# Kernel optimization log

Measured on AMD Instinct MI355X. Metric: run time of the kernel, lower is better.

Reference implementation:

```python
import jax, jax.numpy as jnp
import numpy as np

M_FAI = 1024


def _cmul_mm(a, b):
    # complex matmul of (2, M, M) @ (2, M, M) -> (2, M, M)
    re = a[0] @ b[0] - a[1] @ b[1]
    im = a[0] @ b[1] + a[1] @ b[0]
    return jnp.stack([re, im])


def _cmul_el(a, b):
    # elementwise complex multiply, leading dim 2 = (real, imag)
    re = a[0] * b[0] - a[1] * b[1]
    im = a[0] * b[1] + a[1] * b[0]
    return jnp.stack([re, im])


def _diag(x):
    # diagonal of (2, M, M) -> (2, M)
    return jnp.diagonal(x, axis1=1, axis2=2)


def setup_inputs() -> dict:
    key = jax.random.key(0)
    ks = jax.random.split(key, 13)
    mats = {}
    names = ['Theta', 'A1', 'B1', 'C1', 'A2', 'B2', 'C2', 'A3', 'B3', 'C3']
    for i, n in enumerate(names):
        mats[n] = jax.random.normal(ks[i], (2, M_FAI, M_FAI), dtype=jnp.float32)
    mats['alpha'] = jnp.ones((1,), dtype=jnp.float32)
    mats['belta'] = jnp.ones((1,), dtype=jnp.float32)
    # xavier_uniform with gain=0.01 on (2, M_fai): bound = 0.01*sqrt(6/(2+M_fai))
    bound = 0.01 * np.sqrt(6.0 / (2 + M_FAI))
    mats['param1'] = jax.random.uniform(ks[10], (2, M_FAI), dtype=jnp.float32, minval=-bound, maxval=bound)
    mats['param2'] = jax.random.uniform(ks[11], (2, M_FAI), dtype=jnp.float32, minval=-bound, maxval=bound)
    return mats


def reference(Theta, A1, B1, C1, A2, B2, C2, A3, B3, C3, alpha, belta, param1, param2):
    # approximateTheta = cdiag(param1); diag(p) @ C == columnwise complex scale of C rows
    p = param1[:, :, None]  # (2, M, 1)
    Q1 = _cmul_mm(A1, _cmul_el(p, C1))
    Q2 = _cmul_mm(A2, _cmul_el(p, C2))
    Q3 = _cmul_mm(A2, _cmul_el(p, C3))  # original uses A2 here (faithful)

    Thd = _diag(Theta)  # (2, M)
    b1 = alpha * _cmul_el(_diag(A1), _cmul_el(Thd, _diag(C1))) - _diag(Q1) + _diag(B1)
    b2 = belta * _cmul_el(_diag(A2), _cmul_el(Thd, _diag(C2))) - _diag(Q2) + _diag(B2)
    b3 = belta * _cmul_el(_diag(A3), _cmul_el(Thd, _diag(C3))) - _diag(Q3) + _diag(B3)
    b = b1 + b2 + b3 + param2  # (2, M)
    # per-column complex unit-normalize: torch.norm over the (2,1) column
    norm = jnp.sqrt(jnp.sum(b * b, axis=0, keepdims=True))
    theta_new = b / norm  # (2, M)
    # cdiag: embed as (2, M, M) diagonal complex matrix
    Theta_new = jax.vmap(jnp.diag)(theta_new)
    return Theta_new
```

## Files before the change

kernel.cpp:

```cpp
#include <hip/hip_runtime.h>
#include <math.h>

#define M 1024

#define TI 64
#define KCH 16
#define KSPLIT 16
#define KB (M / KSPLIT)

__global__ __launch_bounds__(256)
void diagq_kernel(const float* __restrict__ A1, const float* __restrict__ C1,
                  const float* __restrict__ A2, const float* __restrict__ C2,
                  const float* __restrict__ C3, const float* __restrict__ p1,
                  float* __restrict__ D )
{
    __shared__ float As_re[TI][KCH + 1];
    __shared__ float As_im[TI][KCH + 1];
    __shared__ float Cs_re[KCH][TI];
    __shared__ float Cs_im[KCH][TI];
    __shared__ float red_re[256];
    __shared__ float red_im[256];

    const int t  = threadIdx.x;
    const int i0 = blockIdx.x * TI;
    const int q  = blockIdx.y;
    const int k0 = blockIdx.z * KB;

    const float* __restrict__ A = (q == 0) ? A1 : A2;
    const float* __restrict__ C = (q == 0) ? C1 : ((q == 1) ? C2 : C3);

    const int i_local = t & 63;
    const int kslice  = t >> 6;

    const int a_ii = t >> 2;
    const int a_kk = (t & 3) << 2;
    const int c_kk = t >> 4;
    const int c_ii = (t & 15) << 2;

    const size_t MM = (size_t)M * M;

    float acc_re = 0.f, acc_im = 0.f;

    for (int s = 0; s < KB / KCH; ++s) {
        const int kbase = k0 + s * KCH;

        {
            const size_t row = (size_t)(i0 + a_ii) * M + kbase + a_kk;
            const float4 are = *(const float4*)(A + row);
            const float4 aim = *(const float4*)(A + MM + row);
            As_re[a_ii][a_kk + 0] = are.x;
            As_re[a_ii][a_kk + 1] = are.y;
            As_re[a_ii][a_kk + 2] = are.z;
            As_re[a_ii][a_kk + 3] = are.w;
            As_im[a_ii][a_kk + 0] = aim.x;
            As_im[a_ii][a_kk + 1] = aim.y;
            As_im[a_ii][a_kk + 2] = aim.z;
            As_im[a_ii][a_kk + 3] = aim.w;
        }
        {
            const int k = kbase + c_kk;
            const float pre = p1[k];
            const float pim = p1[M + k];
            const size_t row = (size_t)k * M + i0 + c_ii;
            const float4 cre = *(const float4*)(C + row);
            const float4 cim = *(const float4*)(C + MM + row);
            Cs_re[c_kk][c_ii + 0] = pre * cre.x - pim * cim.x;
            Cs_re[c_kk][c_ii + 1] = pre * cre.y - pim * cim.y;
            Cs_re[c_kk][c_ii + 2] = pre * cre.z - pim * cim.z;
            Cs_re[c_kk][c_ii + 3] = pre * cre.w - pim * cim.w;
            Cs_im[c_kk][c_ii + 0] = pre * cim.x + pim * cre.x;
            Cs_im[c_kk][c_ii + 1] = pre * cim.y + pim * cre.y;
            Cs_im[c_kk][c_ii + 2] = pre * cim.z + pim * cre.z;
            Cs_im[c_kk][c_ii + 3] = pre * cim.w + pim * cre.w;
        }
        __syncthreads();

        #pragma unroll
        for (int j = 0; j < 4; ++j) {
            const int kk = (kslice << 2) + j;
            const float a_re = As_re[i_local][kk];
            const float a_im = As_im[i_local][kk];
            const float c_re = Cs_re[kk][i_local];
            const float c_im = Cs_im[kk][i_local];
            acc_re += a_re * c_re - a_im * c_im;
            acc_im += a_re * c_im + a_im * c_re;
        }
        __syncthreads();
    }

    red_re[t] = acc_re;
    red_im[t] = acc_im;
    __syncthreads();
    if (t < 64) {
        const float sr = red_re[t] + red_re[t + 64] + red_re[t + 128] + red_re[t + 192];
        const float si = red_im[t] + red_im[t + 64] + red_im[t + 128] + red_im[t + 192];
        atomicAdd(&D[(q * 2 + 0) * M + i0 + t], sr);
        atomicAdd(&D[(q * 2 + 1) * M + i0 + t], si);
    }
}

__global__ __launch_bounds__(256)
void finalize_kernel(const float* __restrict__ Theta,
                     const float* __restrict__ A1, const float* __restrict__ B1, const float* __restrict__ C1,
                     const float* __restrict__ A2, const float* __restrict__ B2, const float* __restrict__ C2,
                     const float* __restrict__ A3, const float* __restrict__ B3, const float* __restrict__ C3,
                     const float* __restrict__ alpha, const float* __restrict__ belta,
                     const float* __restrict__ p2, const float* __restrict__ D,
                     float* __restrict__ out)
{
    const int i = blockIdx.x * blockDim.x + threadIdx.x;
    if (i >= M) return;
    const size_t MM = (size_t)M * M;
    const size_t dg = (size_t)i * M + i;

    const float th_re = Theta[dg], th_im = Theta[MM + dg];
    const float al = alpha[0], be = belta[0];

    float b_re = p2[i], b_im = p2[M + i];

    {
        const float a_re = A1[dg], a_im = A1[MM + dg];
        const float c_re = C1[dg], c_im = C1[MM + dg];
        const float t_re = th_re * c_re - th_im * c_im;
        const float t_im = th_re * c_im + th_im * c_re;
        const float u_re = a_re * t_re - a_im * t_im;
        const float u_im = a_re * t_im + a_im * t_re;
        b_re += al * u_re - D[0 * M + i] + B1[dg];
        b_im += al * u_im - D[1 * M + i] + B1[MM + dg];
    }
    {
        const float a_re = A2[dg], a_im = A2[MM + dg];
        const float c_re = C2[dg], c_im = C2[MM + dg];
        const float t_re = th_re * c_re - th_im * c_im;
        const float t_im = th_re * c_im + th_im * c_re;
        const float u_re = a_re * t_re - a_im * t_im;
        const float u_im = a_re * t_im + a_im * t_re;
        b_re += be * u_re - D[2 * M + i] + B2[dg];
        b_im += be * u_im - D[3 * M + i] + B2[MM + dg];
    }
    {
        const float a_re = A3[dg], a_im = A3[MM + dg];
        const float c_re = C3[dg], c_im = C3[MM + dg];
        const float t_re = th_re * c_re - th_im * c_im;
        const float t_im = th_re * c_im + th_im * c_re;
        const float u_re = a_re * t_re - a_im * t_im;
        const float u_im = a_re * t_im + a_im * t_re;
        b_re += be * u_re - D[4 * M + i] + B3[dg];
        b_im += be * u_im - D[5 * M + i] + B3[MM + dg];
    }

    const float inv = 1.0f / sqrtf(b_re * b_re + b_im * b_im);
    out[dg]      = b_re * inv;
    out[MM + dg] = b_im * inv;
}

extern "C" void kernel_launch(void* const* d_in, const int* in_sizes, int n_in,
                              void* d_out, int out_size, void* d_ws, size_t ws_size,
                              hipStream_t stream) {
    const float* Theta = (const float*)d_in[0];
    const float* A1    = (const float*)d_in[1];
    const float* B1    = (const float*)d_in[2];
    const float* C1    = (const float*)d_in[3];
    const float* A2    = (const float*)d_in[4];
    const float* B2    = (const float*)d_in[5];
    const float* C2    = (const float*)d_in[6];
    const float* A3    = (const float*)d_in[7];
    const float* B3    = (const float*)d_in[8];
    const float* C3    = (const float*)d_in[9];
    const float* alpha = (const float*)d_in[10];
    const float* belta = (const float*)d_in[11];
    const float* p1    = (const float*)d_in[12];
    const float* p2    = (const float*)d_in[13];
    float* out = (float*)d_out;
    float* D   = (float*)d_ws;

    hipMemsetAsync(d_out, 0, (size_t)out_size * sizeof(float), stream);
    hipMemsetAsync(d_ws, 0, 6 * M * sizeof(float), stream);

    dim3 grid(M / TI, 3, KSPLIT);
    diagq_kernel<<<grid, 256, 0, stream>>>(A1, C1, A2, C2, C3, p1, D);

    finalize_kernel<<<dim3(M / 256), 256, 0, stream>>>(
        Theta, A1, B1, C1, A2, B2, C2, A3, B3, C3, alpha, belta, p2, D, out);
}
```

Measured before the change: 136.0 us.

## Fuse output zeroing into finalize, replace atomics with split partials, retile

Removes both hipMemsetAsync calls. The finalize kernel now runs one block per row: it zeroes that row of the output and writes the diagonal element. The diagonal-product kernel writes per-K-split partial sums to the workspace instead of using atomicAdd, and finalize reduces those partials. The tile changes to 32 rows with a K-chunk of 32. This trades launch and memset overhead plus atomics for a larger finalize grid and more workspace traffic.

Measured after the change: 130.5 us. 1.04x faster.

```diff
diff --git a/kernel.cpp b/kernel.cpp
--- a/kernel.cpp
+++ b/kernel.cpp
@@ -3,8 +3,8 @@
 
 #define M 1024
 
-#define TI 64
-#define KCH 16
+#define TI 32
+#define KCH 32
 #define KSPLIT 16
 #define KB (M / KSPLIT)
 
@@ -24,54 +24,50 @@
     const int t  = threadIdx.x;
     const int i0 = blockIdx.x * TI;
     const int q  = blockIdx.y;
-    const int k0 = blockIdx.z * KB;
+    const int z  = blockIdx.z;
+    const int k0 = z * KB;
 
     const float* __restrict__ A = (q == 0) ? A1 : A2;
     const float* __restrict__ C = (q == 0) ? C1 : ((q == 1) ? C2 : C3);
 
-    const int i_local = t & 63;
-    const int kslice  = t >> 6;
-
-    const int a_ii = t >> 2;
-    const int a_kk = (t & 3) << 2;
-    const int c_kk = t >> 4;
-    const int c_ii = (t & 15) << 2;
-
     const size_t MM = (size_t)M * M;
 
+    const int l_row = t >> 3;
+    const int l_c4  = (t & 7) << 2;
+
+    const int i_local = t & 31;
+    const int kslice  = t >> 5;
+
     float acc_re = 0.f, acc_im = 0.f;
 
+    #pragma unroll
     for (int s = 0; s < KB / KCH; ++s) {
         const int kbase = k0 + s * KCH;
 
         {
-            const size_t row = (size_t)(i0 + a_ii) * M + kbase + a_kk;
-            const float4 are = *(const float4*)(A + row);
-            const float4 aim = *(const float4*)(A + MM + row);
-            As_re[a_ii][a_kk + 0] = are.x;
-            As_re[a_ii][a_kk + 1] = are.y;
-            As_re[a_ii][a_kk + 2] = are.z;
-            As_re[a_ii][a_kk + 3] = are.w;
-            As_im[a_ii][a_kk + 0] = aim.x;
-            As_im[a_ii][a_kk + 1] = aim.y;
-            As_im[a_ii][a_kk + 2] = aim.z;
-            As_im[a_ii][a_kk + 3] = aim.w;
-        }
-        {
-            const int k = kbase + c_kk;
+            const size_t off = (size_t)(i0 + l_row) * M + kbase + l_c4;
+            const float4 are = *(const float4*)(A + off);
+            const float4 aim = *(const float4*)(A + MM + off);
+            As_re[l_row][l_c4 + 0] = are.x; As_re[l_row][l_c4 + 1] = are.y;
+            As_re[l_row][l_c4 + 2] = are.z; As_re[l_row][l_c4 + 3] = are.w;
+            As_im[l_row][l_c4 + 0] = aim.x; As_im[l_row][l_c4 + 1] = aim.y;
+            As_im[l_row][l_c4 + 2] = aim.z; As_im[l_row][l_c4 + 3] = aim.w;
+        }
+        {
+            const int k = kbase + l_row;
             const float pre = p1[k];
             const float pim = p1[M + k];
-            const size_t row = (size_t)k * M + i0 + c_ii;
-            const float4 cre = *(const float4*)(C + row);
-            const float4 cim = *(const float4*)(C + MM + row);
-            Cs_re[c_kk][c_ii + 0] = pre * cre.x - pim * cim.x;
-            Cs_re[c_kk][c_ii + 1] = pre * cre.y - pim * cim.y;
-            Cs_re[c_kk][c_ii + 2] = pre * cre.z - pim * cim.z;
-            Cs_re[c_kk][c_ii + 3] = pre * cre.w - pim * cim.w;
-            Cs_im[c_kk][c_ii + 0] = pre * cim.x + pim * cre.x;
-            Cs_im[c_kk][c_ii + 1] = pre * cim.y + pim * cre.y;
-            Cs_im[c_kk][c_ii + 2] = pre * cim.z + pim * cre.z;
-            Cs_im[c_kk][c_ii + 3] = pre * cim.w + pim * cre.w;
+            const size_t off = (size_t)k * M + i0 + l_c4;
+            const float4 cre = *(const float4*)(C + off);
+            const float4 cim = *(const float4*)(C + MM + off);
+            Cs_re[l_row][l_c4 + 0] = pre * cre.x - pim * cim.x;
+            Cs_re[l_row][l_c4 + 1] = pre * cre.y - pim * cim.y;
+            Cs_re[l_row][l_c4 + 2] = pre * cre.z - pim * cim.z;
+            Cs_re[l_row][l_c4 + 3] = pre * cre.w - pim * cim.w;
+            Cs_im[l_row][l_c4 + 0] = pre * cim.x + pim * cre.x;
+            Cs_im[l_row][l_c4 + 1] = pre * cim.y + pim * cre.y;
+            Cs_im[l_row][l_c4 + 2] = pre * cim.z + pim * cre.z;
+            Cs_im[l_row][l_c4 + 3] = pre * cim.w + pim * cre.w;
         }
         __syncthreads();
 
@@ -91,11 +87,12 @@
     red_re[t] = acc_re;
     red_im[t] = acc_im;
     __syncthreads();
-    if (t < 64) {
-        const float sr = red_re[t] + red_re[t + 64] + red_re[t + 128] + red_re[t + 192];
-        const float si = red_im[t] + red_im[t + 64] + red_im[t + 128] + red_im[t + 192];
-        atomicAdd(&D[(q * 2 + 0) * M + i0 + t], sr);
-        atomicAdd(&D[(q * 2 + 1) * M + i0 + t], si);
+    if (t < TI) {
+        float sr = 0.f, si = 0.f;
+        #pragma unroll
+        for (int s = 0; s < 8; ++s) { sr += red_re[t + 32 * s]; si += red_im[t + 32 * s]; }
+        D[((size_t)(q * 2 + 0) * KSPLIT + z) * M + i0 + t] = sr;
+        D[((size_t)(q * 2 + 1) * KSPLIT + z) * M + i0 + t] = si;
     }
 }
 
@@ -108,50 +105,74 @@
                      const float* __restrict__ p2, const float* __restrict__ D,
                      float* __restrict__ out)
 {
-    const int i = blockIdx.x * blockDim.x + threadIdx.x;
-    if (i >= M) return;
+    __shared__ float sv[128];
+
+    const int t = threadIdx.x;
+    const int i = blockIdx.x;
     const size_t MM = (size_t)M * M;
     const size_t dg = (size_t)i * M + i;
 
-    const float th_re = Theta[dg], th_im = Theta[MM + dg];
-    const float al = alpha[0], be = belta[0];
-
-    float b_re = p2[i], b_im = p2[M + i];
-
-    {
-        const float a_re = A1[dg], a_im = A1[MM + dg];
-        const float c_re = C1[dg], c_im = C1[MM + dg];
-        const float t_re = th_re * c_re - th_im * c_im;
-        const float t_im = th_re * c_im + th_im * c_re;
-        const float u_re = a_re * t_re - a_im * t_im;
-        const float u_im = a_re * t_im + a_im * t_re;
-        b_re += al * u_re - D[0 * M + i] + B1[dg];
-        b_im += al * u_im - D[1 * M + i] + B1[MM + dg];
+    if (t < 96) {
+        sv[t] = D[(size_t)t * M + i];
+    } else if (t < 116) {
+        const int j = t - 96;
+        const float* ptrs[10] = {Theta, A1, B1, C1, A2, B2, C2, A3, B3, C3};
+        const float* P = ptrs[j >> 1];
+        sv[t] = P[(j & 1) ? (MM + dg) : dg];
+    } else if (t == 116) { sv[116] = p2[i]; }
+    else if (t == 117)   { sv[117] = p2[M + i]; }
+    else if (t == 118)   { sv[118] = alpha[0]; }
+    else if (t == 119)   { sv[119] = belta[0]; }
+
+    const float4 z4 = make_float4(0.f, 0.f, 0.f, 0.f);
+    ((float4*)(out + (size_t)i * M))[t]      = z4;
+    ((float4*)(out + MM + (size_t)i * M))[t] = z4;
+
+    __syncthreads();
+
+    if (t == 0) {
+        float qs[6];
+        #pragma unroll
+        for (int qc = 0; qc < 6; ++qc) {
+            float s = 0.f;
+            #pragma unroll
+            for (int k = 0; k < 16; ++k) s += sv[qc * 16 + k];
+            qs[qc] = s;
+        }
+        const float th_re = sv[96], th_im = sv[97];
+        const float al = sv[118], be = sv[119];
+
+        float b_re = sv[116], b_im = sv[117];
+
+        {
+            const float a_re = sv[98],  a_im = sv[99];
+            const float c_re = sv[102], c_im = sv[103];
+            const float t_re = th_re * c_re - th_im * c_im;
+            const float t_im = th_re * c_im + th_im * c_re;
+            b_re += al * (a_re * t_re - a_im * t_im) - qs[0] + sv[100];
+            b_im += al * (a_re * t_im + a_im * t_re) - qs[1] + sv[101];
+        }
+        {
+            const float a_re = sv[104], a_im = sv[105];
+            const float c_re = sv[108], c_im = sv[109];
+            const float t_re = th_re * c_re - th_im * c_im;
+            const float t_im = th_re * c_im + th_im * c_re;
+            b_re += be * (a_re * t_re - a_im * t_im) - qs[2] + sv[106];
+            b_im += be * (a_re * t_im + a_im * t_re) - qs[3] + sv[107];
+        }
+        {
+            const float a_re = sv[110], a_im = sv[111];
+            const float c_re = sv[114], c_im = sv[115];
+            const float t_re = th_re * c_re - th_im * c_im;
+            const float t_im = th_re * c_im + th_im * c_re;
+            b_re += be * (a_re * t_re - a_im * t_im) - qs[4] + sv[112];
+            b_im += be * (a_re * t_im + a_im * t_re) - qs[5] + sv[113];
+        }
+
+        const float inv = 1.0f / sqrtf(b_re * b_re + b_im * b_im);
+        out[dg]      = b_re * inv;
+        out[MM + dg] = b_im * inv;
     }
-    {
-        const float a_re = A2[dg], a_im = A2[MM + dg];
-        const float c_re = C2[dg], c_im = C2[MM + dg];
-        const float t_re = th_re * c_re - th_im * c_im;
-        const float t_im = th_re * c_im + th_im * c_re;
-        const float u_re = a_re * t_re - a_im * t_im;
-        const float u_im = a_re * t_im + a_im * t_re;
-        b_re += be * u_re - D[2 * M + i] + B2[dg];
-        b_im += be * u_im - D[3 * M + i] + B2[MM + dg];
-    }
-    {
-        const float a_re = A3[dg], a_im = A3[MM + dg];
-        const float c_re = C3[dg], c_im = C3[MM + dg];
-        const float t_re = th_re * c_re - th_im * c_im;
-        const float t_im = th_re * c_im + th_im * c_re;
-        const float u_re = a_re * t_re - a_im * t_im;
-        const float u_im = a_re * t_im + a_im * t_re;
-        b_re += be * u_re - D[4 * M + i] + B3[dg];
-        b_im += be * u_im - D[5 * M + i] + B3[MM + dg];
-    }
-
-    const float inv = 1.0f / sqrtf(b_re * b_re + b_im * b_im);
-    out[dg]      = b_re * inv;
-    out[MM + dg] = b_im * inv;
 }
 
 extern "C" void kernel_launch(void* const* d_in, const int* in_sizes, int n_in,
@@ -174,12 +195,9 @@
     float* out = (float*)d_out;
     float* D   = (float*)d_ws;
 
-    hipMemsetAsync(d_out, 0, (size_t)out_size * sizeof(float), stream);
-    hipMemsetAsync(d_ws, 0, 6 * M * sizeof(float), stream);
-
     dim3 grid(M / TI, 3, KSPLIT);
     diagq_kernel<<<grid, 256, 0, stream>>>(A1, C1, A2, C2, C3, p1, D);
 
-    finalize_kernel<<<dim3(M / 256), 256, 0, stream>>>(
+    finalize_kernel<<<dim3(M), 256, 0, stream>>>(
         Theta, A1, B1, C1, A2, B2, C2, A3, B3, C3, alpha, belta, p2, D, out);
 }
```
